# Optimization experiments

Measured on AMD Instinct MI355X. Metric: run time of the kernel, lower is better.

The kernel has to match this reference:

```python
import jax, jax.numpy as jnp
import numpy as np

B, T, OBS = 256, 200, 128
H, L, S = 128, 32, 50


def setup_inputs() -> dict:
    key = jax.random.key(0)
    ks = jax.random.split(key, 10)
    sc_in = 1.0 / np.sqrt(OBS + L)
    sc_h = 1.0 / np.sqrt(H)
    return {
        "inputs": jax.random.normal(ks[0], (B, T, OBS), dtype=jnp.float32),
        "eps": jax.random.normal(ks[1], (T, B * S, L), dtype=jnp.float32),
        "W_ih": jax.random.normal(ks[2], (4 * H, OBS + L), dtype=jnp.float32) * sc_in,
        "W_hh": jax.random.normal(ks[3], (4 * H, H), dtype=jnp.float32) * sc_h,
        "b_ih": jax.random.normal(ks[4], (4 * H,), dtype=jnp.float32) * 0.01,
        "b_hh": jax.random.normal(ks[5], (4 * H,), dtype=jnp.float32) * 0.01,
        "W_mu": jax.random.normal(ks[6], (L, H), dtype=jnp.float32) * sc_h,
        "b_mu": jax.random.normal(ks[7], (L,), dtype=jnp.float32) * 0.01,
        "cov_diag": jax.random.uniform(ks[8], (L,), dtype=jnp.float32, minval=0.5, maxval=1.5),
        "num_samples": S,
    }


def reference(inputs, eps, W_ih, W_hh, b_ih, b_hh, W_mu, b_mu, cov_diag, num_samples):
    batch, num_steps, _ = inputs.shape
    hid = b_ih.shape[0] // 4
    lat = b_mu.shape[0]
    BS = batch * num_samples

    std = jnp.sqrt(cov_diag)                       # [L], state-independent diag cov
    logdet = jnp.sum(jnp.log(cov_diag))
    TWO_PI = 2.0 * jnp.pi
    ent_const = 0.5 * lat * (1.0 + jnp.log(TWO_PI)) + 0.5 * logdet

    # tile([num_samples, 1]) in torch repeats the whole batch block -> sample-major
    x_tiled = jnp.tile(inputs.transpose(1, 0, 2), (1, num_samples, 1))  # [T, BS, obs]

    def step(carry, xs):
        h, c, z_prev = carry
        x_t, eps_t = xs
        rnn_in = jnp.concatenate([x_t, z_prev], axis=-1)          # [BS, obs+L]
        gates = rnn_in @ W_ih.T + b_ih + h @ W_hh.T + b_hh        # [BS, 4H]
        i, f, g, o = jnp.split(gates, 4, axis=-1)
        c_new = jax.nn.sigmoid(f) * c + jax.nn.sigmoid(i) * jnp.tanh(g)
        h_new = jax.nn.sigmoid(o) * jnp.tanh(c_new)
        mean = h_new @ W_mu.T + b_mu                              # [BS, L]
        z = mean + eps_t * std                                    # reparam sample
        ent = jnp.broadcast_to(ent_const, (z.shape[0],))          # diag-MVN entropy
        # log N(z; mean, diag(cov)) with (z-mean)/std == eps_t
        lp = -0.5 * (jnp.sum(eps_t * eps_t, axis=-1) + lat * jnp.log(TWO_PI) + logdet)
        return (h_new, c_new, z), (z, ent, lp)

    init = (
        jnp.zeros((BS, hid), dtype=inputs.dtype),
        jnp.zeros((BS, hid), dtype=inputs.dtype),
        jnp.zeros((BS, lat), dtype=inputs.dtype),
    )
    _, (zs, ents, lps) = jax.lax.scan(step, init, (x_tiled, eps))  # [T,BS,L],[T,BS],[T,BS]

    sampled_s = zs.transpose(1, 0, 2).reshape(num_samples, batch, num_steps, lat)
    entropies = ents.T.reshape(num_samples, batch, num_steps)
    log_probs = lps.T.reshape(num_samples, batch, num_steps)
    return sampled_s, entropies, log_probs
```

## Files before the change

### kernel.cpp

```cpp
#include <hip/hip_runtime.h>
#include <stdint.h>

#define T_STEPS 200
#define OBSD    128
#define HID     128
#define LATD    32
#define BS_TOT  12800
#define KIN     160

#define OUT_ENT_OFF 81920000
#define OUT_LP_OFF  84480000

#define WR_OFF  0
#define H_OFF   131072
#define WMU_OFF 147456
#define E_OFF   155648
#define LDS_SZ  159744

#define L2E  1.4426950408889634f
#define L2E2 2.8853900817779268f
#define LOG2PI 1.8378770664093453f

typedef short  bf16x8 __attribute__((ext_vector_type(8)));
typedef float  f32x4  __attribute__((ext_vector_type(4)));
typedef uint32_t u32;

#define BAR() do {                                        \
    __builtin_amdgcn_sched_barrier(0);                    \
    asm volatile("s_waitcnt lgkmcnt(0)" ::: "memory");    \
    __builtin_amdgcn_s_barrier();                         \
    __builtin_amdgcn_sched_barrier(0);                    \
} while (0)

__device__ __forceinline__ uint16_t f2bf(float f) {
    u32 u = __builtin_bit_cast(u32, f);
    u32 r = (u + 0x7fffu + ((u >> 16) & 1u)) >> 16;
    return (uint16_t)r;
}
__device__ __forceinline__ float bf2f(u32 bits16) {
    u32 u = bits16 << 16;
    return __builtin_bit_cast(float, u);
}
__device__ __forceinline__ u32 pack2(float a, float b) {
    return (u32)f2bf(a) | ((u32)f2bf(b) << 16);
}
__device__ __forceinline__ u32 cvt_pk_bf16(float lo, float hi) {
    u32 r;
    asm("v_cvt_pk_bf16_f32 %0, %1, %2" : "=v"(r) : "v"(lo), "v"(hi));
    return r;
}
__device__ __forceinline__ float sig2(float x) {
    float e;
    asm("v_exp_f32 %0, -%1" : "=v"(e) : "v"(x));
    return __builtin_amdgcn_rcpf(1.f + e);
}
__device__ __forceinline__ float tanh2(float x) {
    float e;
    asm("v_exp_f32 %0, %1" : "=v"(e) : "v"(x));
    return 1.f - 2.f * __builtin_amdgcn_rcpf(1.f + e);
}
__device__ __forceinline__ int hswz(int row, int col) {
    return ((row << 8) + (col << 1)) ^ ((row & 7) << 4);
}

__global__ __launch_bounds__(512, 2) void xg_prep(
    const float* __restrict__ x,
    const float* __restrict__ W_ih,
    const float* __restrict__ b_ih,
    const float* __restrict__ b_hh,
    const float* __restrict__ b_mu,
    uint16_t* __restrict__ xg)
{
    const int blk = blockIdx.x;
    const int t   = blk >> 2, bq = blk & 3;
    const int tid = threadIdx.x;
    const int w = tid >> 6, l = tid & 63, lg = l >> 4, ln = l & 15;
    const int b0 = bq * 64;

    bf16x8 wb[4][4];
    float  bias[4];
    #pragma unroll
    for (int q = 0; q < 4; ++q) {
        const int col = q * 128 + w * 16 + ln;
        float zb = 0.f;
        #pragma unroll
        for (int j = 0; j < 32; ++j) zb += b_mu[j] * W_ih[col * KIN + 128 + j];
        bias[q] = b_ih[col] + b_hh[col] + (t > 0 ? zb : 0.f);
        #pragma unroll
        for (int ks = 0; ks < 4; ++ks) {
            bf16x8 v;
            #pragma unroll
            for (int e = 0; e < 8; ++e)
                v[e] = (short)f2bf(W_ih[col * KIN + ks * 32 + lg * 8 + e]);
            wb[ks][q] = v;
        }
    }

    f32x4 acc[4][4];
    const f32x4 vz = {0.f, 0.f, 0.f, 0.f};
    #pragma unroll
    for (int rt = 0; rt < 4; ++rt)
        #pragma unroll
        for (int q = 0; q < 4; ++q) acc[rt][q] = vz;

    #pragma unroll
    for (int ks = 0; ks < 4; ++ks) {
        bf16x8 a[4];
        #pragma unroll
        for (int rt = 0; rt < 4; ++rt) {
            const int brow = b0 + rt * 16 + ln;
            const float* src = x + ((size_t)brow * T_STEPS + t) * OBSD + ks * 32 + lg * 8;
            bf16x8 v;
            #pragma unroll
            for (int e = 0; e < 8; ++e) v[e] = (short)f2bf(src[e]);
            a[rt] = v;
        }
        #pragma unroll
        for (int rt = 0; rt < 4; ++rt)
            #pragma unroll
            for (int q = 0; q < 4; ++q)
                acc[rt][q] = __builtin_amdgcn_mfma_f32_16x16x32_bf16(
                    a[rt], wb[ks][q], acc[rt][q], 0, 0, 0);
    }

    const float gsc[4] = {L2E, L2E, L2E2, L2E};
    uint4* dst = (uint4*)xg + ((size_t)blk * 512 + tid) * 8;
    #pragma unroll
    for (int rt = 0; rt < 4; ++rt) {
        float v0[4], v1[4], v2[4], v3[4];
        #pragma unroll
        for (int e = 0; e < 4; ++e) {
            v0[e] = (acc[rt][0][e] + bias[0]) * gsc[0];
            v1[e] = (acc[rt][1][e] + bias[1]) * gsc[1];
            v2[e] = (acc[rt][2][e] + bias[2]) * gsc[2];
            v3[e] = (acc[rt][3][e] + bias[3]) * gsc[3];
        }
        uint4 o0, o1;
        o0.x = pack2(v0[0], v0[1]); o0.y = pack2(v0[2], v0[3]);
        o0.z = pack2(v1[0], v1[1]); o0.w = pack2(v1[2], v1[3]);
        o1.x = pack2(v2[0], v2[1]); o1.y = pack2(v2[2], v2[3]);
        o1.z = pack2(v3[0], v3[1]); o1.w = pack2(v3[2], v3[3]);
        dst[2 * rt]     = o0;
        dst[2 * rt + 1] = o1;
    }
}

__global__ __launch_bounds__(256) void lp_ent(
    const float* __restrict__ eps,
    const float* __restrict__ cov,
    float* __restrict__ out)
{
    const int blk = blockIdx.x;
    const int rc = blk >> 2, tq = blk & 3;
    const int tid = threadIdx.x;
    const int c = tid & 3, rl = tid >> 2;
    const int row = rc * 64 + rl;

    float logdet = 0.f;
    for (int i = 0; i < LATD; ++i) logdet += logf(cov[i]);
    const float lconst = 32.f * LOG2PI + logdet;
    const float ec = 0.5f * 32.f * (1.f + LOG2PI) + 0.5f * logdet;

    const int t0 = tq * 50;
    for (int t = t0; t < t0 + 50; ++t) {
        const float* ep = eps + ((size_t)t * BS_TOT + row) * LATD + c * 8;
        const float4 a0 = *(const float4*)ep;
        const float4 a1 = *(const float4*)(ep + 4);
        float ps = a0.x*a0.x + a0.y*a0.y + a0.z*a0.z + a0.w*a0.w
                 + a1.x*a1.x + a1.y*a1.y + a1.z*a1.z + a1.w*a1.w;
        ps += __shfl_xor(ps, 1, 64);
        ps += __shfl_xor(ps, 2, 64);
        if (c == 0) {
            out[OUT_LP_OFF  + (size_t)row * 200 + t] = -0.5f * (ps + lconst);
            out[OUT_ENT_OFF + (size_t)row * 200 + t] = ec;
        }
    }
}

__global__ __launch_bounds__(1024, 4) void lstm_main(
    const float* __restrict__ eps,
    const float* __restrict__ W_ih,
    const float* __restrict__ W_hh,
    const float* __restrict__ W_mu,
    const float* __restrict__ b_mu,
    const float* __restrict__ cov,
    const uint16_t* __restrict__ xg,
    float* __restrict__ out)
{
    __shared__ __align__(16) char smem[LDS_SZ];

    const int tid = threadIdx.x;
    const int w = tid >> 6, l = tid & 63, lg = l >> 4, ln = l & 15;
    const int wp = w & 7, half = w >> 3;

    const int xcd = blockIdx.x & 7;
    const int wk  = (xcd >> 1) + 4 * ((blockIdx.x >> 3) + 25 * (xcd & 1));
    const int bq  = wk & 3;
    const int bs0 = wk * 64;

    {
        float* ws = (float*)(smem + H_OFF);
        for (int i = tid; i < 4096; i += 1024) ws[i] = W_mu[i];
    }
    __syncthreads();
    const float* wmu_s = (const float*)(smem + H_OFF);

    for (int i = tid; i < 2048; i += 1024) {
        const int col = i >> 6, k2 = (i & 63) * 2;
        const u32 p = pack2(wmu_s[col * HID + k2], wmu_s[col * HID + k2 + 1]);
        *(u32*)(smem + WMU_OFF + (((col << 8) + (k2 << 1)) ^ ((col & 7) << 4))) = p;
    }

    bf16x8 weg[4];
    {
        float stds[8];
        #pragma unroll
        for (int e = 0; e < 8; ++e) stds[e] = sqrtf(cov[lg * 8 + e]);
        const float gsc[4] = {L2E, L2E, L2E2, L2E};
        #pragma unroll
        for (int q = 0; q < 4; ++q) {
            const int col = q * 128 + wp * 16 + ln;
            bf16x8 v;
            #pragma unroll
            for (int e = 0; e < 8; ++e)
                v[e] = (short)f2bf(W_ih[col * KIN + 128 + lg * 8 + e] * stds[e] * gsc[q]);
            weg[q] = v;
        }
    }

    #pragma unroll
    for (int qq = 0; qq < 2; ++qq) {
        const int q = half * 2 + qq;
        const float gs = (q == 2) ? L2E2 : L2E;
        const int col = q * 128 + wp * 16 + ln;
        float wzf[32];
        #pragma unroll
        for (int j4 = 0; j4 < 8; ++j4)
            *(float4*)&wzf[j4 * 4] = *(const float4*)&W_ih[col * KIN + 128 + j4 * 4];
        #pragma unroll
        for (int ks = 0; ks < 4; ++ks) {
            float base[8];
            *(float4*)&base[0] = *(const float4*)&W_hh[col * HID + ks * 32 + lg * 8];
            *(float4*)&base[4] = *(const float4*)&W_hh[col * HID + ks * 32 + lg * 8 + 4];
            bf16x8 v;
            #pragma unroll
            for (int e = 0; e < 8; ++e) {
                float s = base[e];
                #pragma unroll
                for (int j = 0; j < 32; ++j)
                    s += wzf[j] * wmu_s[j * HID + ks * 32 + lg * 8 + e];
                v[e] = (short)f2bf(s * gs);
            }
            *(bf16x8*)(smem + WR_OFF + (((ks * 4 + q) * 8 + wp) << 10) + l * 16) = v;
        }
    }

    const int rtm = (w >> 1) & 3, ctm = w & 1;
    const int zcol = ctm * 16 + ln;
    const float stdv = sqrtf(cov[zcol]);
    const float bmu  = b_mu[zcol];

    __syncthreads();

    for (int i = tid; i < 4096; i += 1024) ((u32*)(smem + H_OFF))[i] = 0;
    for (int i = tid; i < 1024; i += 1024) ((u32*)(smem + E_OFF))[i] = 0;

    const f32x4 vz4 = {0.f, 0.f, 0.f, 0.f};
    f32x4 cst[2] = {vz4, vz4};

    const int erow = tid >> 4, ecol = (tid & 15) * 2;
    const int ewr = ((erow >> 4) * 64 + (ecol >> 3) * 16 + (erow & 15)) * 16 + (ecol & 7) * 2;

    int hrd[2];
    #pragma unroll
    for (int rt = 0; rt < 2; ++rt)
        hrd[rt] = hswz((half * 2 + rt) * 16 + ln, lg * 8);
    const int wrb = (wp << 10) + l * 16;
    const int egb = E_OFF + ((half * 2) * 64 + l) * 16;

    __syncthreads();

    for (int t = 0; t < T_STEPS; ++t) {
        uint4 xv[4];
        const uint4* xp = (const uint4*)xg
            + ((size_t)(t * 4 + bq) * 512 + wp * 64 + l) * 8 + half * 4;
        #pragma unroll
        for (int i = 0; i < 4; ++i) xv[i] = xp[i];
        const float2 fev = *(const float2*)(eps + ((size_t)t * BS_TOT + bs0 + erow) * LATD + ecol);

        f32x4 acc[2][4];
        bf16x8 aE0 = *(const bf16x8*)(smem + egb);
        bf16x8 aE1 = *(const bf16x8*)(smem + egb + 1024);
        bf16x8 a0[2], b0[4], a1[2], b1[4];
        #pragma unroll
        for (int rt = 0; rt < 2; ++rt)
            a0[rt] = *(const bf16x8*)(smem + H_OFF + hrd[rt]);
        #pragma unroll
        for (int q = 0; q < 4; ++q)
            b0[q] = *(const bf16x8*)(smem + WR_OFF + wrb + q * 8192);
        #pragma unroll
        for (int q = 0; q < 4; ++q) {
            acc[0][q] = __builtin_amdgcn_mfma_f32_16x16x32_bf16(aE0, weg[q], vz4, 0, 0, 0);
            acc[1][q] = __builtin_amdgcn_mfma_f32_16x16x32_bf16(aE1, weg[q], vz4, 0, 0, 0);
        }
        #pragma unroll
        for (int ks = 0; ks < 4; ++ks) {
            if (ks < 3) {
                #pragma unroll
                for (int rt = 0; rt < 2; ++rt)
                    a1[rt] = *(const bf16x8*)(smem + H_OFF + (hrd[rt] ^ 0) + ((hswz((half*2+rt)*16+ln, (ks+1)*32 + lg*8)) - hrd[rt]));
                #pragma unroll
                for (int q = 0; q < 4; ++q)
                    b1[q] = *(const bf16x8*)(smem + WR_OFF + wrb + ((ks + 1) * 4 + q) * 8192);
            }
            #pragma unroll
            for (int rt = 0; rt < 2; ++rt)
                #pragma unroll
                for (int q = 0; q < 4; ++q)
                    acc[rt][q] = __builtin_amdgcn_mfma_f32_16x16x32_bf16(
                        a0[rt], b0[q], acc[rt][q], 0, 0, 0);
            #pragma unroll
            for (int rt = 0; rt < 2; ++rt) a0[rt] = a1[rt];
            #pragma unroll
            for (int q = 0; q < 4; ++q) b0[q] = b1[q];
        }
        if (half == 0 && t > 0) {
            f32x4 macc = vz4;
            #pragma unroll
            for (int ks = 0; ks < 4; ++ks) {
                const bf16x8 am = *(const bf16x8*)(smem + H_OFF + hswz(rtm * 16 + ln, ks * 32 + lg * 8));
                const bf16x8 bm = *(const bf16x8*)(smem + WMU_OFF + hswz(zcol, ks * 32 + lg * 8));
                macc = __builtin_amdgcn_mfma_f32_16x16x32_bf16(am, bm, macc, 0, 0, 0);
            }
            #pragma unroll
            for (int e = 0; e < 4; ++e) {
                const int row = rtm * 16 + lg * 4 + e;
                const int eb = (rtm * 64 + (zcol >> 3) * 16 + (lg * 4 + e)) * 16 + (zcol & 7) * 2;
                const float evv = bf2f(*(const uint16_t*)(smem + E_OFF + eb));
                out[(size_t)(bs0 + row) * 6400 + (t - 1) * 32 + zcol] =
                    macc[e] + bmu + evv * stdv;
            }
        }

        BAR();

        *(u32*)(smem + E_OFF + ewr) = cvt_pk_bf16(fev.x, fev.y);

        #pragma unroll
        for (int rt = 0; rt < 2; ++rt) {
            const uint4 u01 = xv[2 * rt], u23 = xv[2 * rt + 1];
            const float xi[4] = { bf2f(u01.x & 0xffff), bf2f(u01.x >> 16),
                                  bf2f(u01.y & 0xffff), bf2f(u01.y >> 16) };
            const float xf[4] = { bf2f(u01.z & 0xffff), bf2f(u01.z >> 16),
                                  bf2f(u01.w & 0xffff), bf2f(u01.w >> 16) };
            const float xgv[4] = { bf2f(u23.x & 0xffff), bf2f(u23.x >> 16),
                                   bf2f(u23.y & 0xffff), bf2f(u23.y >> 16) };
            const float xo[4] = { bf2f(u23.z & 0xffff), bf2f(u23.z >> 16),
                                  bf2f(u23.w & 0xffff), bf2f(u23.w >> 16) };
            #pragma unroll
            for (int e = 0; e < 4; ++e) {
                const float iv = acc[rt][0][e] + xi[e];
                const float fv = acc[rt][1][e] + xf[e];
                const float gv = acc[rt][2][e] + xgv[e];
                const float ov = acc[rt][3][e] + xo[e];
                const float c  = sig2(fv) * cst[rt][e] + sig2(iv) * tanh2(gv);
                cst[rt][e] = c;
                const float h = sig2(ov) * tanh2(c * L2E2);
                const int row = (half * 2 + rt) * 16 + lg * 4 + e;
                *(uint16_t*)(smem + H_OFF + hswz(row, wp * 16 + ln)) = f2bf(h);
            }
        }

        BAR();
    }

    if (half == 0) {
        f32x4 macc = vz4;
        #pragma unroll
        for (int ks = 0; ks < 4; ++ks) {
            const bf16x8 am = *(const bf16x8*)(smem + H_OFF + hswz(rtm * 16 + ln, ks * 32 + lg * 8));
            const bf16x8 bm = *(const bf16x8*)(smem + WMU_OFF + hswz(zcol, ks * 32 + lg * 8));
            macc = __builtin_amdgcn_mfma_f32_16x16x32_bf16(am, bm, macc, 0, 0, 0);
        }
        #pragma unroll
        for (int e = 0; e < 4; ++e) {
            const int row = rtm * 16 + lg * 4 + e;
            const int eb = (rtm * 64 + (zcol >> 3) * 16 + (lg * 4 + e)) * 16 + (zcol & 7) * 2;
            const float evv = bf2f(*(const uint16_t*)(smem + E_OFF + eb));
            out[(size_t)(bs0 + row) * 6400 + 199 * 32 + zcol] =
                macc[e] + bmu + evv * stdv;
        }
    }
}

extern "C" void kernel_launch(void* const* d_in, const int* in_sizes, int n_in,
                              void* d_out, int out_size, void* d_ws, size_t ws_size,
                              hipStream_t stream) {
    const float* x    = (const float*)d_in[0];
    const float* eps  = (const float*)d_in[1];
    const float* W_ih = (const float*)d_in[2];
    const float* W_hh = (const float*)d_in[3];
    const float* b_ih = (const float*)d_in[4];
    const float* b_hh = (const float*)d_in[5];
    const float* W_mu = (const float*)d_in[6];
    const float* b_mu = (const float*)d_in[7];
    const float* cov  = (const float*)d_in[8];
    float* out = (float*)d_out;
    uint16_t* xg = (uint16_t*)d_ws;

    hipLaunchKernelGGL(xg_prep, dim3(800), dim3(512), 0, stream, x, W_ih, b_ih, b_hh, b_mu, xg);
    hipLaunchKernelGGL(lp_ent, dim3(800), dim3(256), 0, stream, eps, cov, out);
    hipLaunchKernelGGL(lstm_main, dim3(200), dim3(1024), 0, stream,
                       eps, W_ih, W_hh, W_mu, b_mu, cov, xg, out);
}
```

Baseline: 1.482 ms.

## Fuse lp/entropy into LSTM launch, prefetch xg, seed MFMA accumulators

Removes the separate lp_ent kernel and runs its work in 56 extra blocks of the LSTM launch, using otherwise idle CUs alongside the 200 recurrent blocks. The precomputed input-gate values for the next step are prefetched one iteration ahead and used directly as the MFMA accumulator seed, so the per-element bf16 adds after the matmul go away. The h write packs pairs with cvt_pk_bf16. The extra blocks read eps with a per-thread stride pattern that coalesces less well than before and compete for memory bandwidth with the recurrent blocks.

Result: slower. 2.038 ms (+37.5%).

```diff
diff --git a/kernel.cpp b/kernel.cpp
--- a/kernel.cpp
+++ b/kernel.cpp
@@ -61,6 +61,14 @@
 }
 __device__ __forceinline__ int hswz(int row, int col) {
     return ((row << 8) + (col << 1)) ^ ((row & 7) << 4);
+}
+__device__ __forceinline__ f32x4 cfrag(u32 u01, u32 u23) {
+    f32x4 c;
+    c[0] = __builtin_bit_cast(float, u01 << 16);
+    c[1] = __builtin_bit_cast(float, u01 & 0xffff0000u);
+    c[2] = __builtin_bit_cast(float, u23 << 16);
+    c[3] = __builtin_bit_cast(float, u23 & 0xffff0000u);
+    return c;
 }
 
 __global__ __launch_bounds__(512, 2) void xg_prep(
@@ -145,38 +153,6 @@
     }
 }
 
-__global__ __launch_bounds__(256) void lp_ent(
-    const float* __restrict__ eps,
-    const float* __restrict__ cov,
-    float* __restrict__ out)
-{
-    const int blk = blockIdx.x;
-    const int rc = blk >> 2, tq = blk & 3;
-    const int tid = threadIdx.x;
-    const int c = tid & 3, rl = tid >> 2;
-    const int row = rc * 64 + rl;
-
-    float logdet = 0.f;
-    for (int i = 0; i < LATD; ++i) logdet += logf(cov[i]);
-    const float lconst = 32.f * LOG2PI + logdet;
-    const float ec = 0.5f * 32.f * (1.f + LOG2PI) + 0.5f * logdet;
-
-    const int t0 = tq * 50;
-    for (int t = t0; t < t0 + 50; ++t) {
-        const float* ep = eps + ((size_t)t * BS_TOT + row) * LATD + c * 8;
-        const float4 a0 = *(const float4*)ep;
-        const float4 a1 = *(const float4*)(ep + 4);
-        float ps = a0.x*a0.x + a0.y*a0.y + a0.z*a0.z + a0.w*a0.w
-                 + a1.x*a1.x + a1.y*a1.y + a1.z*a1.z + a1.w*a1.w;
-        ps += __shfl_xor(ps, 1, 64);
-        ps += __shfl_xor(ps, 2, 64);
-        if (c == 0) {
-            out[OUT_LP_OFF  + (size_t)row * 200 + t] = -0.5f * (ps + lconst);
-            out[OUT_ENT_OFF + (size_t)row * 200 + t] = ec;
-        }
-    }
-}
-
 __global__ __launch_bounds__(1024, 4) void lstm_main(
     const float* __restrict__ eps,
     const float* __restrict__ W_ih,
@@ -190,6 +166,32 @@
     __shared__ __align__(16) char smem[LDS_SZ];
 
     const int tid = threadIdx.x;
+
+    if (blockIdx.x >= 200) {
+        const int row = (blockIdx.x - 200) * 1024 + tid;
+        if (row < BS_TOT) {
+            float logdet = 0.f;
+            for (int i = 0; i < LATD; ++i) logdet += logf(cov[i]);
+            const float lconst = 32.f * LOG2PI + logdet;
+            const float ec = 0.5f * 32.f * (1.f + LOG2PI) + 0.5f * logdet;
+            const float* ep0 = eps + (size_t)row * LATD;
+            float* lpw = out + OUT_LP_OFF  + (size_t)row * 200;
+            float* enw = out + OUT_ENT_OFF + (size_t)row * 200;
+            for (int t = 0; t < T_STEPS; ++t) {
+                const float* ep = ep0 + (size_t)t * BS_TOT * LATD;
+                float ps = 0.f;
+                #pragma unroll
+                for (int k = 0; k < 8; ++k) {
+                    const float4 a = *(const float4*)(ep + k * 4);
+                    ps += a.x * a.x + a.y * a.y + a.z * a.z + a.w * a.w;
+                }
+                lpw[t] = -0.5f * (ps + lconst);
+                enw[t] = ec;
+            }
+        }
+        return;
+    }
+
     const int w = tid >> 6, l = tid & 63, lg = l >> 4, ln = l & 15;
     const int wp = w & 7, half = w >> 3;
 
@@ -271,44 +273,60 @@
     const int erow = tid >> 4, ecol = (tid & 15) * 2;
     const int ewr = ((erow >> 4) * 64 + (ecol >> 3) * 16 + (erow & 15)) * 16 + (ecol & 7) * 2;
 
-    int hrd[2];
-    #pragma unroll
-    for (int rt = 0; rt < 2; ++rt)
-        hrd[rt] = hswz((half * 2 + rt) * 16 + ln, lg * 8);
     const int wrb = (wp << 10) + l * 16;
     const int egb = E_OFF + ((half * 2) * 64 + l) * 16;
 
+    uint4 xvp[4];
+    {
+        const uint4* xp = (const uint4*)xg
+            + ((size_t)(0 * 4 + bq) * 512 + wp * 64 + l) * 8 + half * 4;
+        #pragma unroll
+        for (int i = 0; i < 4; ++i) xvp[i] = xp[i];
+    }
+
     __syncthreads();
 
     for (int t = 0; t < T_STEPS; ++t) {
-        uint4 xv[4];
-        const uint4* xp = (const uint4*)xg
-            + ((size_t)(t * 4 + bq) * 512 + wp * 64 + l) * 8 + half * 4;
-        #pragma unroll
-        for (int i = 0; i < 4; ++i) xv[i] = xp[i];
+        f32x4 acc[2][4];
+        #pragma unroll
+        for (int rt = 0; rt < 2; ++rt) {
+            const uint4 ua = xvp[2 * rt], ub = xvp[2 * rt + 1];
+            acc[rt][0] = cfrag(ua.x, ua.y);
+            acc[rt][1] = cfrag(ua.z, ua.w);
+            acc[rt][2] = cfrag(ub.x, ub.y);
+            acc[rt][3] = cfrag(ub.z, ub.w);
+        }
+
+        const int tn = (t + 1 < T_STEPS) ? t + 1 : t;
+        {
+            const uint4* xp = (const uint4*)xg
+                + ((size_t)(tn * 4 + bq) * 512 + wp * 64 + l) * 8 + half * 4;
+            #pragma unroll
+            for (int i = 0; i < 4; ++i) xvp[i] = xp[i];
+        }
         const float2 fev = *(const float2*)(eps + ((size_t)t * BS_TOT + bs0 + erow) * LATD + ecol);
 
-        f32x4 acc[2][4];
-        bf16x8 aE0 = *(const bf16x8*)(smem + egb);
-        bf16x8 aE1 = *(const bf16x8*)(smem + egb + 1024);
+        const bf16x8 aE0 = *(const bf16x8*)(smem + egb);
+        const bf16x8 aE1 = *(const bf16x8*)(smem + egb + 1024);
         bf16x8 a0[2], b0[4], a1[2], b1[4];
         #pragma unroll
         for (int rt = 0; rt < 2; ++rt)
-            a0[rt] = *(const bf16x8*)(smem + H_OFF + hrd[rt]);
+            a0[rt] = *(const bf16x8*)(smem + H_OFF + hswz((half * 2 + rt) * 16 + ln, lg * 8));
         #pragma unroll
         for (int q = 0; q < 4; ++q)
             b0[q] = *(const bf16x8*)(smem + WR_OFF + wrb + q * 8192);
         #pragma unroll
         for (int q = 0; q < 4; ++q) {
-            acc[0][q] = __builtin_amdgcn_mfma_f32_16x16x32_bf16(aE0, weg[q], vz4, 0, 0, 0);
-            acc[1][q] = __builtin_amdgcn_mfma_f32_16x16x32_bf16(aE1, weg[q], vz4, 0, 0, 0);
+            acc[0][q] = __builtin_amdgcn_mfma_f32_16x16x32_bf16(aE0, weg[q], acc[0][q], 0, 0, 0);
+            acc[1][q] = __builtin_amdgcn_mfma_f32_16x16x32_bf16(aE1, weg[q], acc[1][q], 0, 0, 0);
         }
         #pragma unroll
         for (int ks = 0; ks < 4; ++ks) {
             if (ks < 3) {
                 #pragma unroll
                 for (int rt = 0; rt < 2; ++rt)
-                    a1[rt] = *(const bf16x8*)(smem + H_OFF + (hrd[rt] ^ 0) + ((hswz((half*2+rt)*16+ln, (ks+1)*32 + lg*8)) - hrd[rt]));
+                    a1[rt] = *(const bf16x8*)(smem + H_OFF
+                        + hswz((half * 2 + rt) * 16 + ln, (ks + 1) * 32 + lg * 8));
                 #pragma unroll
                 for (int q = 0; q < 4; ++q)
                     b1[q] = *(const bf16x8*)(smem + WR_OFF + wrb + ((ks + 1) * 4 + q) * 8192);
@@ -335,8 +353,8 @@
             #pragma unroll
             for (int e = 0; e < 4; ++e) {
                 const int row = rtm * 16 + lg * 4 + e;
-                const int eb = (rtm * 64 + (zcol >> 3) * 16 + (lg * 4 + e)) * 16 + (zcol & 7) * 2;
-                const float evv = bf2f(*(const uint16_t*)(smem + E_OFF + eb));
+                const float evv = bf2f(*(const uint16_t*)(
+                    smem + E_OFF + ((rtm * 64 + (zcol >> 3) * 16 + (lg * 4 + e)) << 4) + (zcol & 7) * 2));
                 out[(size_t)(bs0 + row) * 6400 + (t - 1) * 32 + zcol] =
                     macc[e] + bmu + evv * stdv;
             }
@@ -348,27 +366,22 @@
 
         #pragma unroll
         for (int rt = 0; rt < 2; ++rt) {
-            const uint4 u01 = xv[2 * rt], u23 = xv[2 * rt + 1];
-            const float xi[4] = { bf2f(u01.x & 0xffff), bf2f(u01.x >> 16),
-                                  bf2f(u01.y & 0xffff), bf2f(u01.y >> 16) };
-            const float xf[4] = { bf2f(u01.z & 0xffff), bf2f(u01.z >> 16),
-                                  bf2f(u01.w & 0xffff), bf2f(u01.w >> 16) };
-            const float xgv[4] = { bf2f(u23.x & 0xffff), bf2f(u23.x >> 16),
-                                   bf2f(u23.y & 0xffff), bf2f(u23.y >> 16) };
-            const float xo[4] = { bf2f(u23.z & 0xffff), bf2f(u23.z >> 16),
-                                  bf2f(u23.w & 0xffff), bf2f(u23.w >> 16) };
+            float hv[4];
             #pragma unroll
             for (int e = 0; e < 4; ++e) {
-                const float iv = acc[rt][0][e] + xi[e];
-                const float fv = acc[rt][1][e] + xf[e];
-                const float gv = acc[rt][2][e] + xgv[e];
-                const float ov = acc[rt][3][e] + xo[e];
-                const float c  = sig2(fv) * cst[rt][e] + sig2(iv) * tanh2(gv);
+                const float c = sig2(acc[rt][1][e]) * cst[rt][e]
+                              + sig2(acc[rt][0][e]) * tanh2(acc[rt][2][e]);
                 cst[rt][e] = c;
-                const float h = sig2(ov) * tanh2(c * L2E2);
-                const int row = (half * 2 + rt) * 16 + lg * 4 + e;
-                *(uint16_t*)(smem + H_OFF + hswz(row, wp * 16 + ln)) = f2bf(h);
-            }
+                hv[e] = sig2(acc[rt][3][e]) * tanh2(c * L2E2);
+            }
+            const u32 p01 = cvt_pk_bf16(hv[0], hv[1]);
+            const u32 p23 = cvt_pk_bf16(hv[2], hv[3]);
+            const int r0 = (half * 2 + rt) * 16 + lg * 4;
+            const int hc = wp * 16 + ln;
+            *(uint16_t*)(smem + H_OFF + hswz(r0,     hc)) = (uint16_t)p01;
+            *(uint16_t*)(smem + H_OFF + hswz(r0 + 1, hc)) = (uint16_t)(p01 >> 16);
+            *(uint16_t*)(smem + H_OFF + hswz(r0 + 2, hc)) = (uint16_t)p23;
+            *(uint16_t*)(smem + H_OFF + hswz(r0 + 3, hc)) = (uint16_t)(p23 >> 16);
         }
 
         BAR();
@@ -385,8 +398,8 @@
         #pragma unroll
         for (int e = 0; e < 4; ++e) {
             const int row = rtm * 16 + lg * 4 + e;
-            const int eb = (rtm * 64 + (zcol >> 3) * 16 + (lg * 4 + e)) * 16 + (zcol & 7) * 2;
-            const float evv = bf2f(*(const uint16_t*)(smem + E_OFF + eb));
+            const float evv = bf2f(*(const uint16_t*)(
+                smem + E_OFF + ((rtm * 64 + (zcol >> 3) * 16 + (lg * 4 + e)) << 4) + (zcol & 7) * 2));
             out[(size_t)(bs0 + row) * 6400 + 199 * 32 + zcol] =
                 macc[e] + bmu + evv * stdv;
         }
@@ -409,7 +422,6 @@
     uint16_t* xg = (uint16_t*)d_ws;
 
     hipLaunchKernelGGL(xg_prep, dim3(800), dim3(512), 0, stream, x, W_ih, b_ih, b_hh, b_mu, xg);
-    hipLaunchKernelGGL(lp_ent, dim3(800), dim3(256), 0, stream, eps, cov, out);
-    hipLaunchKernelGGL(lstm_main, dim3(200), dim3(1024), 0, stream,
+    hipLaunchKernelGGL(lstm_main, dim3(256), dim3(1024), 0, stream,
                        eps, W_ih, W_hh, W_mu, b_mu, cov, xg, out);
 }
```
